# Performance work log

Measured on AMD Instinct MI355X. Metric: run time of the kernel, lower is better.

## Reference

```python
import jax, jax.numpy as jnp
import numpy as np

B, T, E, H = 8, 2048, 1024, 64

def setup_inputs() -> dict:
    key = jax.random.key(0)
    kx, kk, kq, kv = jax.random.split(key, 4)
    x = jax.random.normal(kx, (B, T, E), dtype=jnp.float32)
    # nn.Linear weight init scale ~ 1/sqrt(fan_in); use small normal weights
    s = 1.0 / np.sqrt(E)
    Wk = jax.random.normal(kk, (E, H), dtype=jnp.float32) * s
    Wq = jax.random.normal(kq, (E, H), dtype=jnp.float32) * s
    Wv = jax.random.normal(kv, (E, H), dtype=jnp.float32) * s
    return {"x": x, "Wk": Wk, "Wq": Wq, "Wv": Wv}

def reference(x, Wk, Wq, Wv):
    # x: [B,T,E]; projections to head_size H
    k = jnp.einsum('bte,eh->bth', x, Wk)
    q = jnp.einsum('bte,eh->bth', x, Wq)
    v = jnp.einsum('bte,eh->bth', x, Wv)
    # NOTE: original scales by num_embds**-0.5 (E, not head_size)
    scale = jnp.asarray(E, x.dtype) ** -0.5
    wei = jnp.einsum('bqh,bkh->bqk', q, k) * scale  # [B,T,T]
    causal = jnp.tril(jnp.ones((T, T), dtype=bool))
    wei = jnp.where(causal, wei, -jnp.inf)
    wei = jax.nn.softmax(wei, axis=-1)
    # dropout p=0.0 -> identity (eval-mode deterministic baseline)
    out = jnp.einsum('bqk,bkh->bqh', wei, v)  # [B,T,H]
    return out
```

## Files before the change

### kernel.cpp

```cpp
#include <hip/hip_runtime.h>
#include <hip/hip_bf16.h>

#define B_ 8
#define T_ 2048
#define E_ 1024
#define H_ 64

typedef __attribute__((ext_vector_type(8))) short short8v;
typedef __attribute__((ext_vector_type(4))) float f32x4;

__device__ __forceinline__ unsigned short bfbits(float f) {
  return __builtin_bit_cast(unsigned short, __float2bfloat16(f));
}

__device__ __forceinline__ void gload_lds16(const void* g, void* l) {
  __builtin_amdgcn_global_load_lds(
      (const __attribute__((address_space(1))) unsigned*)g,
      (__attribute__((address_space(3))) unsigned*)l, 16, 0, 0);
}

__global__ __launch_bounds__(256) void prep_wt(
    const float* __restrict__ Wk, const float* __restrict__ Wq,
    const float* __restrict__ Wv, __hip_bfloat16* __restrict__ Wt) {
  const int idx = blockIdx.x * 256 + threadIdx.x;
  const int k = idx & 1023;
  const int c = (idx >> 10) & 63;
  const int m = idx >> 16;
  const float* W = (m == 0) ? Wk : (m == 1) ? Wq : Wv;
  float v = W[k * H_ + c];
  if (m == 1) v *= 0.03125f;
  Wt[idx] = __float2bfloat16(v);
}

__global__ __launch_bounds__(256) void proj_mfma(
    const float* __restrict__ x, const __hip_bfloat16* __restrict__ Wt,
    __hip_bfloat16* __restrict__ Qb, __hip_bfloat16* __restrict__ Kb,
    __hip_bfloat16* __restrict__ Vt) {
  __shared__ float xs[3][32][64];
  __shared__ __hip_bfloat16 Ws[2][192][64];
  __shared__ __hip_bfloat16 rep[4][32][24];
  const int tid = threadIdx.x;
  const int lane = tid & 63;
  const int w = tid >> 6;
  const int r = lane & 15, g = lane >> 4;
  const int r0 = blockIdx.x * 32;

  f32x4 acc[3][2];
  #pragma unroll
  for (int m = 0; m < 3; ++m)
    #pragma unroll
    for (int rt = 0; rt < 2; ++rt) acc[m][rt] = (f32x4){0.f, 0.f, 0.f, 0.f};

  auto stageX = [&](int buf, int kc) {
    #pragma unroll
    for (int jj = 0; jj < 2; ++jj) {
      const int jb = w * 2 + jj;
      const int row = jb * 4 + (lane >> 4);
      const int sl = lane & 15;
      const int ssl = (sl & 8) | ((sl & 7) ^ (row & 7));
      gload_lds16(x + (size_t)(r0 + row) * E_ + kc + ssl * 4, &xs[buf][jb * 4][0]);
    }
  };
  auto stageW = [&](int buf, int kc) {
    #pragma unroll
    for (int jj = 0; jj < 6; ++jj) {
      const int jb = w * 6 + jj;
      const int row = jb * 8 + (lane >> 3);
      const int sl = (lane & 7) ^ (row & 7);
      gload_lds16(Wt + (size_t)row * E_ + kc + sl * 8, &Ws[buf][jb * 8][0]);
    }
  };

  auto compute = [&](int bx, int bw) {
    #pragma unroll
    for (int kh = 0; kh < 2; ++kh) {
      short8v a[2];
      #pragma unroll
      for (int rt = 0; rt < 2; ++rt) {
        const int row = rt * 16 + r;
        const char* base = (const char*)&xs[bx][0][0] + row * 256;
        const int s0 = kh * 8 + ((2 * g + 0) ^ (r & 7));
        const int s1 = kh * 8 + ((2 * g + 1) ^ (r & 7));
        const f32x4 lo = *(const f32x4*)(base + s0 * 16);
        const f32x4 hi = *(const f32x4*)(base + s1 * 16);
        short8v t8;
        t8[0] = (short)bfbits(lo[0]); t8[1] = (short)bfbits(lo[1]);
        t8[2] = (short)bfbits(lo[2]); t8[3] = (short)bfbits(lo[3]);
        t8[4] = (short)bfbits(hi[0]); t8[5] = (short)bfbits(hi[1]);
        t8[6] = (short)bfbits(hi[2]); t8[7] = (short)bfbits(hi[3]);
        a[rt] = t8;
      }
      #pragma unroll
      for (int m = 0; m < 3; ++m) {
        const int rowW = m * 64 + w * 16 + r;
        const int sl = (kh * 4 + g) ^ (r & 7);
        const short8v bf =
            *(const short8v*)((const char*)&Ws[bw][0][0] + rowW * 128 + sl * 16);
        #pragma unroll
        for (int rt = 0; rt < 2; ++rt)
          acc[m][rt] = __builtin_amdgcn_mfma_f32_16x16x32_bf16(a[rt], bf, acc[m][rt], 0, 0, 0);
      }
    }
  };

  stageX(0, 0);
  __builtin_amdgcn_sched_barrier(0);
  stageW(0, 0);
  __builtin_amdgcn_sched_barrier(0);
  stageX(1, 64);
  asm volatile("s_waitcnt vmcnt(2)" ::: "memory");
  __builtin_amdgcn_s_barrier();

  #pragma unroll
  for (int t = 0; t < 16; ++t) {
    if (t + 1 < 16) stageW((t + 1) & 1, (t + 1) * 64);
    __builtin_amdgcn_sched_barrier(0);
    if (t + 2 < 16) stageX((t + 2) % 3, (t + 2) * 64);
    __builtin_amdgcn_sched_barrier(0);
    compute(t % 3, t & 1);
    if (t + 2 < 16) {
      asm volatile("s_waitcnt vmcnt(2)" ::: "memory");
    } else if (t + 1 < 16) {
      asm volatile("s_waitcnt vmcnt(0)" ::: "memory");
    }
    if (t + 1 < 16) __builtin_amdgcn_s_barrier();
  }

  __hip_bfloat16* rp = &rep[w][0][0];
  #pragma unroll
  for (int m = 0; m < 2; ++m) {
    __hip_bfloat16* Pout = (m == 0) ? Kb : Qb;
    #pragma unroll
    for (int rt = 0; rt < 2; ++rt)
      #pragma unroll
      for (int reg = 0; reg < 4; ++reg)
        rp[(rt * 16 + g * 4 + reg) * 24 + r] = __float2bfloat16(acc[m][rt][reg]);
    asm volatile("s_waitcnt lgkmcnt(0)" ::: "memory");
    __builtin_amdgcn_sched_barrier(0);
    {
      const int row = lane >> 1, ch = lane & 1;
      *(uint4*)(Pout + (size_t)(r0 + row) * H_ + w * 16 + ch * 8) =
          *(const uint4*)(rp + row * 24 + ch * 8);
    }
    asm volatile("s_waitcnt lgkmcnt(0)" ::: "memory");
    __builtin_amdgcn_sched_barrier(0);
  }
  const int b = r0 >> 11;
  const int tt = r0 & 2047;
  #pragma unroll
  for (int rt = 0; rt < 2; ++rt) {
    ushort4 pk;
    pk.x = bfbits(acc[2][rt][0]); pk.y = bfbits(acc[2][rt][1]);
    pk.z = bfbits(acc[2][rt][2]); pk.w = bfbits(acc[2][rt][3]);
    *(ushort4*)(Vt + (size_t)(b * 64 + w * 16 + r) * T_ + tt + rt * 16 + g * 4) = pk;
  }
}

__global__ __launch_bounds__(128, 2) void attn_mfma(
    const __hip_bfloat16* __restrict__ Qb, const __hip_bfloat16* __restrict__ Kb,
    const __hip_bfloat16* __restrict__ Vt, float* __restrict__ out) {
  __shared__ __hip_bfloat16 Ps[2][16][72];
  __shared__ float cmb[64][20];
  __shared__ float ml[16][2];
  const int tid = threadIdx.x;
  const int lane = tid & 63;
  const int w = tid >> 6;
  const int r = lane & 15, g = lane >> 4;
  const int blk = blockIdx.x;
  const int b = blk & 7;
  const int i = blk >> 3;
  const int s_ = i >> 5, j_ = i & 31;
  const int qt = (s_ == 0) ? j_ : (s_ == 1) ? (63 - j_) : (s_ == 2) ? (64 + j_) : (127 - j_);
  const int q0 = qt * 16;
  const size_t tb = (size_t)b * T_;
  const int bb = b * 64;

  const short8v qf0 = *(const short8v*)(Qb + (tb + q0 + r) * H_ + g * 8);
  const short8v qf1 = *(const short8v*)(Qb + (tb + q0 + r) * H_ + 32 + g * 8);

  f32x4 o[4];
  #pragma unroll
  for (int k2 = 0; k2 < 4; ++k2) o[k2] = (f32x4){0.f, 0.f, 0.f, 0.f};
  float mrun = -1e30f, lrun = 0.f;

  const int nt = (qt >> 2) + 1;
  const int h_ = (nt + 1) >> 1;
  const int t0 = w ? h_ : 0;
  const int t1 = w ? nt : h_;

  short8v kbA[4][2], kbB[4][2];
  auto loadK = [&](int t, short8v (&kb)[4][2]) {
    #pragma unroll
    for (int kg = 0; kg < 4; ++kg)
      #pragma unroll
      for (int c = 0; c < 2; ++c)
        kb[kg][c] = *(const short8v*)(Kb + (tb + t * 64 + kg * 16 + r) * H_ + c * 32 + g * 8);
  };

  auto body = [&](int t, short8v (&kbU)[4][2], short8v (&kbP)[4][2]) {
    short8v vb[4][2];
    #pragma unroll
    for (int hg = 0; hg < 4; ++hg)
      #pragma unroll
      for (int c = 0; c < 2; ++c)
        vb[hg][c] = *(const short8v*)(
            Vt + (size_t)(bb + hg * 16 + r) * T_ + t * 64 + c * 32 + g * 8);
    if (t + 1 < t1) loadK(t + 1, kbP);

    f32x4 s[4];
    #pragma unroll
    for (int k2 = 0; k2 < 4; ++k2) s[k2] = (f32x4){0.f, 0.f, 0.f, 0.f};
    __builtin_amdgcn_s_setprio(1);
    #pragma unroll
    for (int kg = 0; kg < 4; ++kg) {
      s[kg] = __builtin_amdgcn_mfma_f32_16x16x32_bf16(kbU[kg][0], qf0, s[kg], 0, 0, 0);
      s[kg] = __builtin_amdgcn_mfma_f32_16x16x32_bf16(kbU[kg][1], qf1, s[kg], 0, 0, 0);
    }
    __builtin_amdgcn_s_setprio(0);

    if (t == nt - 1) {
      #pragma unroll
      for (int kg = 0; kg < 4; ++kg)
        #pragma unroll
        for (int reg = 0; reg < 4; ++reg)
          if (t * 64 + kg * 16 + g * 4 + reg > q0 + r) s[kg][reg] = -1e30f;
    }

    float pm = s[0][0];
    #pragma unroll
    for (int kg = 0; kg < 4; ++kg)
      #pragma unroll
      for (int reg = 0; reg < 4; ++reg) pm = fmaxf(pm, s[kg][reg]);
    pm = fmaxf(pm, __shfl_xor(pm, 16));
    pm = fmaxf(pm, __shfl_xor(pm, 32));
    const float nm = fmaxf(mrun, pm);
    const float al = __expf(mrun - nm);
    mrun = nm;
    float p[4][4];
    float rs = 0.f;
    #pragma unroll
    for (int kg = 0; kg < 4; ++kg)
      #pragma unroll
      for (int reg = 0; reg < 4; ++reg) {
        p[kg][reg] = __expf(s[kg][reg] - nm);
        rs += p[kg][reg];
      }
    rs += __shfl_xor(rs, 16);
    rs += __shfl_xor(rs, 32);
    lrun = lrun * al + rs;
    #pragma unroll
    for (int hg = 0; hg < 4; ++hg) o[hg] *= al;

    #pragma unroll
    for (int kg = 0; kg < 4; ++kg) {
      ushort4 u;
      u.x = bfbits(p[kg][0]); u.y = bfbits(p[kg][1]);
      u.z = bfbits(p[kg][2]); u.w = bfbits(p[kg][3]);
      *(ushort4*)&Ps[w][r][kg * 16 + g * 4] = u;
    }
    short8v pf[2];
    pf[0] = *(const short8v*)&Ps[w][r][g * 8];
    pf[1] = *(const short8v*)&Ps[w][r][32 + g * 8];

    __builtin_amdgcn_s_setprio(1);
    #pragma unroll
    for (int c = 0; c < 2; ++c)
      #pragma unroll
      for (int hg = 0; hg < 4; ++hg)
        o[hg] = __builtin_amdgcn_mfma_f32_16x16x32_bf16(vb[hg][c], pf[c], o[hg], 0, 0, 0);
    __builtin_amdgcn_s_setprio(0);
  };

  if (t0 < t1) {
    loadK(t0, kbA);
    int t = t0;
    while (true) {
      body(t, kbA, kbB);
      if (++t >= t1) break;
      body(t, kbB, kbA);
      if (++t >= t1) break;
    }
  }

  if (w == 1) {
    if (g == 0) { ml[r][0] = mrun; ml[r][1] = lrun; }
    #pragma unroll
    for (int hg = 0; hg < 4; ++hg) *(f32x4*)&cmb[lane][hg * 4] = o[hg];
  }
  __syncthreads();
  if (w == 0) {
    const float m1 = ml[r][0], l1 = ml[r][1];
    const float mm = fmaxf(mrun, m1);
    const float sc0 = __expf(mrun - mm), sc1 = __expf(m1 - mm);
    const float inv = 1.f / (lrun * sc0 + l1 * sc1);
    #pragma unroll
    for (int hg = 0; hg < 4; ++hg) {
      const f32x4 o1 = *(const f32x4*)&cmb[lane][hg * 4];
      f32x4 res = (o[hg] * sc0 + o1 * sc1) * inv;
      *(f32x4*)(out + (tb + q0 + r) * H_ + hg * 16 + g * 4) = res;
    }
  }
}

extern "C" void kernel_launch(void* const* d_in, const int* in_sizes, int n_in,
                              void* d_out, int out_size, void* d_ws, size_t ws_size,
                              hipStream_t stream) {
  const float* x  = (const float*)d_in[0];
  const float* Wk = (const float*)d_in[1];
  const float* Wq = (const float*)d_in[2];
  const float* Wv = (const float*)d_in[3];
  float* out = (float*)d_out;

  __hip_bfloat16* Qb = (__hip_bfloat16*)d_ws;
  __hip_bfloat16* Kb = Qb + (size_t)B_ * T_ * H_;
  __hip_bfloat16* Vt = Kb + (size_t)B_ * T_ * H_;
  __hip_bfloat16* Wt = Vt + (size_t)B_ * T_ * H_;

  prep_wt<<<(3 * H_ * E_) / 256, 256, 0, stream>>>(Wk, Wq, Wv, Wt);
  proj_mfma<<<(B_ * T_) / 32, 256, 0, stream>>>(x, Wt, Qb, Kb, Vt);
  attn_mfma<<<B_ * (T_ / 16), 128, 0, stream>>>(Qb, Kb, Vt, out);
}
```

Before: 59.68 us.

## Widen projection tiles to 64 rows and split attention KV across four waves

The projection kernel now runs 512-thread blocks covering 64 rows, so each staged W tile is shared by twice as many rows, which halves total W traffic. The attention kernel now splits each query tile's key range across four waves instead of two and merges the partial softmax states through shared memory. This shortens the per-block serial KV loop, which matters most for the long late query tiles. In exchange it costs more LDS, a larger merge step, lower occupancy limits for the projection, and idle waves on short tiles.

```diff
diff --git a/kernel.cpp b/kernel.cpp
--- a/kernel.cpp
+++ b/kernel.cpp
@@ -32,18 +32,21 @@
   Wt[idx] = __float2bfloat16(v);
 }
 
-__global__ __launch_bounds__(256) void proj_mfma(
+__global__ __launch_bounds__(512) void proj_mfma(
     const float* __restrict__ x, const __hip_bfloat16* __restrict__ Wt,
     __hip_bfloat16* __restrict__ Qb, __hip_bfloat16* __restrict__ Kb,
     __hip_bfloat16* __restrict__ Vt) {
-  __shared__ float xs[3][32][64];
+  __shared__ float xs[3][64][64];
   __shared__ __hip_bfloat16 Ws[2][192][64];
-  __shared__ __hip_bfloat16 rep[4][32][24];
+  __shared__ __hip_bfloat16 rep[8][32][24];
   const int tid = threadIdx.x;
   const int lane = tid & 63;
   const int w = tid >> 6;
+  const int rowg = w >> 2;
+  const int colg = w & 3;
   const int r = lane & 15, g = lane >> 4;
-  const int r0 = blockIdx.x * 32;
+  const int r0 = blockIdx.x * 64;
+  const int rw0 = r0 + rowg * 32;
 
   f32x4 acc[3][2];
   #pragma unroll
@@ -54,20 +57,20 @@
   auto stageX = [&](int buf, int kc) {
     #pragma unroll
     for (int jj = 0; jj < 2; ++jj) {
-      const int jb = w * 2 + jj;
-      const int row = jb * 4 + (lane >> 4);
+      const int rr = w * 8 + jj * 4 + (lane >> 4);
       const int sl = lane & 15;
-      const int ssl = (sl & 8) | ((sl & 7) ^ (row & 7));
-      gload_lds16(x + (size_t)(r0 + row) * E_ + kc + ssl * 4, &xs[buf][jb * 4][0]);
+      const int ssl = (sl & 8) | ((sl & 7) ^ (rr & 7));
+      gload_lds16(x + (size_t)(r0 + rr) * E_ + kc + ssl * 4,
+                  &xs[buf][w * 8 + jj * 4][0]);
     }
   };
   auto stageW = [&](int buf, int kc) {
     #pragma unroll
-    for (int jj = 0; jj < 6; ++jj) {
-      const int jb = w * 6 + jj;
-      const int row = jb * 8 + (lane >> 3);
-      const int sl = (lane & 7) ^ (row & 7);
-      gload_lds16(Wt + (size_t)row * E_ + kc + sl * 8, &Ws[buf][jb * 8][0]);
+    for (int jj = 0; jj < 3; ++jj) {
+      const int jb = w * 3 + jj;
+      const int rr = jb * 8 + (lane >> 3);
+      const int sl = (lane & 7) ^ (rr & 7);
+      gload_lds16(Wt + (size_t)rr * E_ + kc + sl * 8, &Ws[buf][jb * 8][0]);
     }
   };
 
@@ -77,7 +80,7 @@
       short8v a[2];
       #pragma unroll
       for (int rt = 0; rt < 2; ++rt) {
-        const int row = rt * 16 + r;
+        const int row = rowg * 32 + rt * 16 + r;
         const char* base = (const char*)&xs[bx][0][0] + row * 256;
         const int s0 = kh * 8 + ((2 * g + 0) ^ (r & 7));
         const int s1 = kh * 8 + ((2 * g + 1) ^ (r & 7));
@@ -92,7 +95,7 @@
       }
       #pragma unroll
       for (int m = 0; m < 3; ++m) {
-        const int rowW = m * 64 + w * 16 + r;
+        const int rowW = m * 64 + colg * 16 + r;
         const int sl = (kh * 4 + g) ^ (r & 7);
         const short8v bf =
             *(const short8v*)((const char*)&Ws[bw][0][0] + rowW * 128 + sl * 16);
@@ -116,7 +119,6 @@
     if (t + 1 < 16) stageW((t + 1) & 1, (t + 1) * 64);
     __builtin_amdgcn_sched_barrier(0);
     if (t + 2 < 16) stageX((t + 2) % 3, (t + 2) * 64);
-    __builtin_amdgcn_sched_barrier(0);
     compute(t % 3, t & 1);
     if (t + 2 < 16) {
       asm volatile("s_waitcnt vmcnt(2)" ::: "memory");
@@ -139,29 +141,29 @@
     __builtin_amdgcn_sched_barrier(0);
     {
       const int row = lane >> 1, ch = lane & 1;
-      *(uint4*)(Pout + (size_t)(r0 + row) * H_ + w * 16 + ch * 8) =
+      *(uint4*)(Pout + (size_t)(rw0 + row) * H_ + colg * 16 + ch * 8) =
           *(const uint4*)(rp + row * 24 + ch * 8);
     }
     asm volatile("s_waitcnt lgkmcnt(0)" ::: "memory");
     __builtin_amdgcn_sched_barrier(0);
   }
   const int b = r0 >> 11;
-  const int tt = r0 & 2047;
+  const int tt = rw0 & 2047;
   #pragma unroll
   for (int rt = 0; rt < 2; ++rt) {
     ushort4 pk;
     pk.x = bfbits(acc[2][rt][0]); pk.y = bfbits(acc[2][rt][1]);
     pk.z = bfbits(acc[2][rt][2]); pk.w = bfbits(acc[2][rt][3]);
-    *(ushort4*)(Vt + (size_t)(b * 64 + w * 16 + r) * T_ + tt + rt * 16 + g * 4) = pk;
-  }
-}
-
-__global__ __launch_bounds__(128, 2) void attn_mfma(
+    *(ushort4*)(Vt + (size_t)(b * 64 + colg * 16 + r) * T_ + tt + rt * 16 + g * 4) = pk;
+  }
+}
+
+__global__ __launch_bounds__(256, 4) void attn_mfma(
     const __hip_bfloat16* __restrict__ Qb, const __hip_bfloat16* __restrict__ Kb,
     const __hip_bfloat16* __restrict__ Vt, float* __restrict__ out) {
-  __shared__ __hip_bfloat16 Ps[2][16][72];
-  __shared__ float cmb[64][20];
-  __shared__ float ml[16][2];
+  __shared__ __hip_bfloat16 Ps[4][16][72];
+  __shared__ float cmb[3][64][20];
+  __shared__ float ml[3][16][2];
   const int tid = threadIdx.x;
   const int lane = tid & 63;
   const int w = tid >> 6;
@@ -184,9 +186,9 @@
   float mrun = -1e30f, lrun = 0.f;
 
   const int nt = (qt >> 2) + 1;
-  const int h_ = (nt + 1) >> 1;
-  const int t0 = w ? h_ : 0;
-  const int t1 = w ? nt : h_;
+  const int qc = nt >> 2, rem = nt & 3;
+  const int t0 = w * qc + (w < rem ? w : rem);
+  const int t1 = t0 + qc + (w < rem ? 1 : 0);
 
   short8v kbA[4][2], kbB[4][2];
   auto loadK = [&](int t, short8v (&kb)[4][2]) {
@@ -282,23 +284,33 @@
     }
   }
 
-  if (w == 1) {
-    if (g == 0) { ml[r][0] = mrun; ml[r][1] = lrun; }
-    #pragma unroll
-    for (int hg = 0; hg < 4; ++hg) *(f32x4*)&cmb[lane][hg * 4] = o[hg];
+  if (w > 0) {
+    if (g == 0) { ml[w - 1][r][0] = mrun; ml[w - 1][r][1] = lrun; }
+    #pragma unroll
+    for (int hg = 0; hg < 4; ++hg) *(f32x4*)&cmb[w - 1][lane][hg * 4] = o[hg];
   }
   __syncthreads();
   if (w == 0) {
-    const float m1 = ml[r][0], l1 = ml[r][1];
-    const float mm = fmaxf(mrun, m1);
-    const float sc0 = __expf(mrun - mm), sc1 = __expf(m1 - mm);
-    const float inv = 1.f / (lrun * sc0 + l1 * sc1);
-    #pragma unroll
-    for (int hg = 0; hg < 4; ++hg) {
-      const f32x4 o1 = *(const f32x4*)&cmb[lane][hg * 4];
-      f32x4 res = (o[hg] * sc0 + o1 * sc1) * inv;
-      *(f32x4*)(out + (tb + q0 + r) * H_ + hg * 16 + g * 4) = res;
-    }
+    float mm = mrun;
+    #pragma unroll
+    for (int j = 0; j < 3; ++j) mm = fmaxf(mm, ml[j][r][0]);
+    const float sc = __expf(mrun - mm);
+    float l = lrun * sc;
+    f32x4 oo[4];
+    #pragma unroll
+    for (int hg = 0; hg < 4; ++hg) oo[hg] = o[hg] * sc;
+    #pragma unroll
+    for (int j = 0; j < 3; ++j) {
+      const float scj = __expf(ml[j][r][0] - mm);
+      l += ml[j][r][1] * scj;
+      #pragma unroll
+      for (int hg = 0; hg < 4; ++hg)
+        oo[hg] += *(const f32x4*)&cmb[j][lane][hg * 4] * scj;
+    }
+    const float inv = 1.f / l;
+    #pragma unroll
+    for (int hg = 0; hg < 4; ++hg)
+      *(f32x4*)(out + (tb + q0 + r) * H_ + hg * 16 + g * 4) = oo[hg] * inv;
   }
 }
 
@@ -317,6 +329,6 @@
   __hip_bfloat16* Wt = Vt + (size_t)B_ * T_ * H_;
 
   prep_wt<<<(3 * H_ * E_) / 256, 256, 0, stream>>>(Wk, Wq, Wv, Wt);
-  proj_mfma<<<(B_ * T_) / 32, 256, 0, stream>>>(x, Wt, Qb, Kb, Vt);
-  attn_mfma<<<B_ * (T_ / 16), 128, 0, stream>>>(Qb, Kb, Vt, out);
-}
+  proj_mfma<<<(B_ * T_) / 64, 512, 0, stream>>>(x, Wt, Qb, Kb, Vt);
+  attn_mfma<<<B_ * (T_ / 16), 256, 0, stream>>>(Qb, Kb, Vt, out);
+}
```

After: 95.79 us. 60.5% more time.
